# Optimization experiments

Measured on AMD Instinct MI355X. Metric: run time of the kernel, lower is better.

The kernel has to match this reference:

```python
import jax, jax.numpy as jnp
import numpy as np

K = 20  # neighbors per point
EPS = 1e-5


def knn_idx(x, k):
    # x: (B,C,N) -> indices of k nearest neighbors (B,N,k), largest negative sq-dist
    xx = jnp.sum(x * x, axis=1)                      # (B,N)
    inner = jnp.einsum('bcn,bcm->bnm', x, x)         # (B,N,N)
    neg_dist = 2.0 * inner - xx[:, :, None] - xx[:, None, :]
    return jax.lax.top_k(neg_dist, k)[1]             # (B,N,k)


def graph_feature(x, k):
    # x: (B,C,N) -> (B,2C,N,k) = cat(neighbor - center, center)
    idx = knn_idx(x, k)
    gather = jax.vmap(lambda xb, ib: xb[:, ib])(x, idx)      # (B,C,N,k)
    center = jnp.broadcast_to(x[:, :, :, None], gather.shape)
    return jnp.concatenate([gather - center, center], axis=1)


def bn(x, g, b, axes):
    # training-mode batchnorm over given axes; channel axis = 1
    m = jnp.mean(x, axis=axes, keepdims=True)
    v = jnp.var(x, axis=axes, keepdims=True)
    sh = [1] * x.ndim
    sh[1] = x.shape[1]
    return (x - m) * jax.lax.rsqrt(v + EPS) * g.reshape(sh) + b.reshape(sh)


def lrelu(x):
    return jnp.where(x >= 0, x, 0.2 * x)


def edge_block(x, W, g, b, k):
    # EdgeConv: knn-gather -> 1x1 conv -> BN -> LeakyReLU -> max over k
    f = graph_feature(x, k)                          # (B,2C,N,k)
    y = jnp.einsum('oc,bcnk->bonk', W, f)
    return jnp.max(lrelu(bn(y, g, b, (0, 2, 3))), axis=-1)   # (B,O,N)


def conv1d_bn(x, W, g, b):
    y = jnp.einsum('oc,bcn->bon', W, x)
    return lrelu(bn(y, g, b, (0, 2)))


def setup_inputs() -> dict:
    key = jax.random.key(0)
    ks = jax.random.split(key, 12)
    B, N = 4, 4096
    d = {'points': jax.random.normal(ks[0], (B, N, 3), dtype=jnp.float32)}

    def w(k, o, c):
        return jax.random.normal(k, (o, c), dtype=jnp.float32) * (1.0 / np.sqrt(c))

    d['W1'] = w(ks[1], 64, 6);     d['g1'] = jnp.ones(64);  d['b1'] = jnp.zeros(64)
    d['W2'] = w(ks[2], 64, 128);   d['g2'] = jnp.ones(64);  d['b2'] = jnp.zeros(64)
    d['W3'] = w(ks[3], 128, 128);  d['g3'] = jnp.ones(128); d['b3'] = jnp.zeros(128)
    d['W4'] = w(ks[4], 256, 256);  d['g4'] = jnp.ones(256); d['b4'] = jnp.zeros(256)
    d['W5'] = w(ks[5], 512, 512);  d['g5'] = jnp.ones(512); d['b5'] = jnp.zeros(512)
    d['Ws1'] = w(ks[6], 256, 1024); d['gs1'] = jnp.ones(256); d['bs1'] = jnp.zeros(256)
    d['Ws2'] = w(ks[7], 128, 256);  d['gs2'] = jnp.ones(128); d['bs2'] = jnp.zeros(128)
    d['Ws3'] = w(ks[8], 2, 128);    d['bias3'] = jnp.zeros(2)
    return d


def reference(points, W1, g1, b1, W2, g2, b2, W3, g3, b3, W4, g4, b4,
              W5, g5, b5, Ws1, gs1, bs1, Ws2, gs2, bs2, Ws3, bias3):
    x = jnp.transpose(points, (0, 2, 1))             # (B,3,N)
    x1 = edge_block(x, W1, g1, b1, K)                # (B,64,N)
    x2 = edge_block(x1, W2, g2, b2, K)               # (B,64,N)
    x3 = edge_block(x2, W3, g3, b3, K)               # (B,128,N)
    x4 = edge_block(x3, W4, g4, b4, K)               # (B,256,N)
    xc = jnp.concatenate([x1, x2, x3, x4], axis=1)   # (B,512,N)
    x5 = conv1d_bn(xc, W5, g5, b5)                   # (B,512,N)
    g = jnp.broadcast_to(jnp.max(x5, axis=2, keepdims=True), x5.shape)
    feat = jnp.concatenate([xc, g], axis=1)          # (B,1024,N)
    h = conv1d_bn(feat, Ws1, gs1, bs1)               # (B,256,N)
    h = conv1d_bn(h, Ws2, gs2, bs2)                  # (B,128,N)
    return jnp.einsum('oc,bcn->bon', Ws3, h) + bias3[None, :, None]  # (B,2,N)
```

## Files before the change

kernel.cpp:

```cpp
#include <hip/hip_runtime.h>

#define NPTS 4096
#define NB 4
#define KNN 20
#define NCAND 64
#define RANKT 32
#define MROWS (NB*NPTS)

__device__ __forceinline__ float lrelu(float v) { return v >= 0.f ? v : 0.2f * v; }

__device__ __forceinline__ unsigned fkey(float f) {
  unsigned u = __float_as_uint(f);
  return (u & 0x80000000u) ? ~u : (u | 0x80000000u);
}
__device__ __forceinline__ float funkey(unsigned k) {
  unsigned u = (k & 0x80000000u) ? (k ^ 0x80000000u) : ~k;
  return __uint_as_float(u);
}

__global__ __launch_bounds__(256) void sqnorm_k(const float* __restrict__ X, int ldx, int C,
                                                float* __restrict__ xx) {
  int r = blockIdx.x * 256 + threadIdx.x;
  if (r >= MROWS) return;
  const float* row = X + (size_t)r * ldx;
  float s = 0.f;
  for (int c = 0; c < C; ++c) { float v = row[c]; s += v * v; }
  xx[r] = s;
}

__global__ __launch_bounds__(256, 2) void gemm128_k(
    const float* __restrict__ A, int lda,
    const float* __restrict__ B, int ldb, int C,
    float* __restrict__ out, int ldo,
    const float* __restrict__ bias2d, int bstride,
    const float* __restrict__ xxa, const float* __restrict__ xxb) {
  __shared__ float As[32][128];
  __shared__ float Bs[32][128];
  int t = threadIdx.x;
  int tx = t & 15, ty = t >> 4;
  int mbase = blockIdx.x * 128;
  int rbase = blockIdx.y * 128;
  float acc[8][8] = {};
  int lr = t >> 1;
  int lk = (t & 1) * 16;
  const float* pa0 = A + (size_t)(rbase + lr) * lda + lk;
  const float* pb0 = B + (size_t)(mbase + lr) * ldb + lk;
  for (int kc = 0; kc < C; kc += 32) {
    const float* pa = pa0 + kc;
    const float* pb = pb0 + kc;
    #pragma unroll
    for (int j4 = 0; j4 < 4; ++j4) {
      float4 a4 = *(const float4*)(pa + j4 * 4);
      float4 b4 = *(const float4*)(pb + j4 * 4);
      As[lk + j4*4 + 0][lr] = a4.x;
      As[lk + j4*4 + 1][lr] = a4.y;
      As[lk + j4*4 + 2][lr] = a4.z;
      As[lk + j4*4 + 3][lr] = a4.w;
      Bs[lk + j4*4 + 0][lr] = b4.x;
      Bs[lk + j4*4 + 1][lr] = b4.y;
      Bs[lk + j4*4 + 2][lr] = b4.z;
      Bs[lk + j4*4 + 3][lr] = b4.w;
    }
    __syncthreads();
    #pragma unroll
    for (int k = 0; k < 32; ++k) {
      float4 a0 = ((const float4*)As[k])[ty];
      float4 a1 = ((const float4*)As[k])[16 + ty];
      float4 b0 = ((const float4*)Bs[k])[tx];
      float4 b1 = ((const float4*)Bs[k])[16 + tx];
      float av[8] = {a0.x,a0.y,a0.z,a0.w,a1.x,a1.y,a1.z,a1.w};
      float bv[8] = {b0.x,b0.y,b0.z,b0.w,b1.x,b1.y,b1.z,b1.w};
      #pragma unroll
      for (int i = 0; i < 8; ++i)
        #pragma unroll
        for (int j = 0; j < 8; ++j)
          acc[i][j] += av[i] * bv[j];
    }
    __syncthreads();
  }
  #pragma unroll
  for (int ih = 0; ih < 2; ++ih) {
    #pragma unroll
    for (int i4 = 0; i4 < 4; ++i4) {
      int i = ih * 4 + i4;
      int r = rbase + ih * 64 + ty * 4 + i4;
      float xr = xxa ? xxa[r] : 0.f;
      const float* brow = bias2d ? (bias2d + (size_t)(r >> 12) * bstride) : nullptr;
      #pragma unroll
      for (int jh = 0; jh < 2; ++jh) {
        float4 o4;
        #pragma unroll
        for (int j4 = 0; j4 < 4; ++j4) {
          int j = jh * 4 + j4;
          int m = mbase + jh * 64 + tx * 4 + j4;
          float val = acc[i][j];
          if (xxa) val = 2.f * val - xr - xxb[m];
          else if (brow) val += brow[m];
          (&o4.x)[j4] = val;
        }
        *(float4*)&out[(size_t)r * ldo + mbase + jh * 64 + tx * 4] = o4;
      }
    }
  }
}

__global__ __launch_bounds__(256, 2) void dist_tri_k(const float* __restrict__ Xb, int ldx, int C,
                                                     const float* __restrict__ xxb,
                                                     float* __restrict__ D) {
  __shared__ float As[32][128];
  __shared__ float Bs[32][128];
  __shared__ float Ts[32][129];
  int t = threadIdx.x;
  int tx = t & 15, ty = t >> 4;
  int lin = blockIdx.x, bi = 0;
  while (lin >= 32 - bi) { lin -= 32 - bi; ++bi; }
  int bj = bi + lin;
  int rbase = bi * 128;
  int mbase = bj * 128;
  float acc[8][8] = {};
  int lr = t >> 1;
  int lk = (t & 1) * 16;
  const float* pa0 = Xb + (size_t)(rbase + lr) * ldx + lk;
  const float* pb0 = Xb + (size_t)(mbase + lr) * ldx + lk;
  for (int kc = 0; kc < C; kc += 32) {
    const float* pa = pa0 + kc;
    const float* pb = pb0 + kc;
    #pragma unroll
    for (int j4 = 0; j4 < 4; ++j4) {
      float4 a4 = *(const float4*)(pa + j4 * 4);
      float4 b4 = *(const float4*)(pb + j4 * 4);
      As[lk + j4*4 + 0][lr] = a4.x;
      As[lk + j4*4 + 1][lr] = a4.y;
      As[lk + j4*4 + 2][lr] = a4.z;
      As[lk + j4*4 + 3][lr] = a4.w;
      Bs[lk + j4*4 + 0][lr] = b4.x;
      Bs[lk + j4*4 + 1][lr] = b4.y;
      Bs[lk + j4*4 + 2][lr] = b4.z;
      Bs[lk + j4*4 + 3][lr] = b4.w;
    }
    __syncthreads();
    #pragma unroll
    for (int k = 0; k < 32; ++k) {
      float4 a0 = ((const float4*)As[k])[ty];
      float4 a1 = ((const float4*)As[k])[16 + ty];
      float4 b0 = ((const float4*)Bs[k])[tx];
      float4 b1 = ((const float4*)Bs[k])[16 + tx];
      float av[8] = {a0.x,a0.y,a0.z,a0.w,a1.x,a1.y,a1.z,a1.w};
      float bv[8] = {b0.x,b0.y,b0.z,b0.w,b1.x,b1.y,b1.z,b1.w};
      #pragma unroll
      for (int i = 0; i < 8; ++i)
        #pragma unroll
        for (int j = 0; j < 8; ++j)
          acc[i][j] += av[i] * bv[j];
    }
    __syncthreads();
  }
  #pragma unroll
  for (int ih = 0; ih < 2; ++ih) {
    #pragma unroll
    for (int i4 = 0; i4 < 4; ++i4) {
      int i = ih * 4 + i4;
      int r = rbase + ih * 64 + ty * 4 + i4;
      float xr = xxb[r];
      #pragma unroll
      for (int jh = 0; jh < 2; ++jh) {
        float4 o4;
        #pragma unroll
        for (int j4 = 0; j4 < 4; ++j4) {
          int j = jh * 4 + j4;
          int m = mbase + jh * 64 + tx * 4 + j4;
          float val = 2.f * acc[i][j] - xr - xxb[m];
          acc[i][j] = val;
          (&o4.x)[j4] = val;
        }
        *(float4*)&D[(size_t)r * NPTS + mbase + jh * 64 + tx * 4] = o4;
      }
    }
  }
  if (bi != bj) {
    #pragma unroll
    for (int g = 0; g < 4; ++g) {
      __syncthreads();
      #pragma unroll
      for (int jh = 0; jh < 2; ++jh) {
        int mlo = jh * 64 + tx * 4;
        if ((mlo >> 5) == g) {
          #pragma unroll
          for (int i = 0; i < 8; ++i) {
            int r_local = (i >> 2) * 64 + ty * 4 + (i & 3);
            #pragma unroll
            for (int j4 = 0; j4 < 4; ++j4)
              Ts[(mlo & 31) + j4][r_local] = acc[i][jh * 4 + j4];
          }
        }
      }
      __syncthreads();
      int rowg = t >> 3;
      int colb = (t & 7) * 16;
      int mg = mbase + g * 32 + rowg;
      float4* dst = (float4*)&D[(size_t)mg * NPTS + rbase + colb];
      #pragma unroll
      for (int q = 0; q < 4; ++q) {
        float4 vq;
        vq.x = Ts[rowg][colb + q*4 + 0];
        vq.y = Ts[rowg][colb + q*4 + 1];
        vq.z = Ts[rowg][colb + q*4 + 2];
        vq.w = Ts[rowg][colb + q*4 + 3];
        dst[q] = vq;
      }
    }
  }
}

#define HISTN (16*257)

__global__ __launch_bounds__(256) void select_k(const float* __restrict__ D,
                                                int* __restrict__ cand, int b, int n0) {
  __shared__ __align__(16) unsigned keys[NPTS];
  __shared__ __align__(16) int hist[HISTN];
  __shared__ int wtot[4];
  __shared__ unsigned sT;
  __shared__ unsigned sM;
  __shared__ int sR;
  __shared__ int sA;
  __shared__ int sDone;
  __shared__ int sCnt;
  int t = threadIdx.x;
  int wv = t >> 6;
  int lane = t & 63;
  int* hrow = hist + (t & 15) * 257;
  int r = blockIdx.x;
  const float4* drow4 = (const float4*)(D + (size_t)r * NPTS);
  int4 z4 = {0, 0, 0, 0};
  #pragma unroll
  for (int i = 0; i < HISTN/4/256 + 1; ++i) {
    int idx = i * 256 + t;
    if (idx < HISTN/4) ((int4*)hist)[idx] = z4;
  }
  if (t == 0) { sT = 0u; sM = 0u; sR = RANKT; sA = 0; sDone = 0; sCnt = 0; }
  __syncthreads();
  #pragma unroll
  for (int i = 0; i < 4; ++i) {
    float4 d4 = drow4[i*256 + t];
    uint4 k4;
    k4.x = fkey(d4.x); k4.y = fkey(d4.y); k4.z = fkey(d4.z); k4.w = fkey(d4.w);
    ((uint4*)keys)[i*256 + t] = k4;
    atomicAdd(&hrow[k4.x >> 24], 1);
    atomicAdd(&hrow[k4.y >> 24], 1);
    atomicAdd(&hrow[k4.z >> 24], 1);
    atomicAdd(&hrow[k4.w >> 24], 1);
  }
  __syncthreads();
  int done = 0;
  for (int level = 0; level < 4 && !done; ++level) {
    unsigned M = sM, T = sT;
    int R = sR;
    int shift = 24 - 8 * level;
    if (level > 0) {
      #pragma unroll
      for (int i = 0; i < HISTN/4/256 + 1; ++i) {
        int idx = i * 256 + t;
        if (idx < HISTN/4) ((int4*)hist)[idx] = z4;
      }
      __syncthreads();
      #pragma unroll
      for (int i = 0; i < 4; ++i) {
        uint4 k4 = ((uint4*)keys)[i*256 + t];
        if ((k4.x & M) == T) atomicAdd(&hrow[(k4.x >> shift) & 0xffu], 1);
        if ((k4.y & M) == T) atomicAdd(&hrow[(k4.y >> shift) & 0xffu], 1);
        if ((k4.z & M) == T) atomicAdd(&hrow[(k4.z >> shift) & 0xffu], 1);
        if ((k4.w & M) == T) atomicAdd(&hrow[(k4.w >> shift) & 0xffu], 1);
      }
      __syncthreads();
    }
    int h = 0;
    #pragma unroll
    for (int j = 0; j < 16; ++j) h += hist[j * 257 + t];
    int s = h;
    #pragma unroll
    for (int off = 1; off < 64; off <<= 1) {
      int o = __shfl(s, lane + off);
      if (lane + off < 64) s += o;
    }
    if (lane == 0) wtot[wv] = s;
    __syncthreads();
    int aw = 0;
    for (int w = wv + 1; w < 4; ++w) aw += wtot[w];
    int sAbove = (s - h) + aw;
    if (sAbove < R && R <= sAbove + h) {
      unsigned v = (unsigned)t;
      int strictNow = sA + sAbove;
      sT = T | (v << shift);
      sM = M | (0xffu << shift);
      sA = strictNow;
      sR = R - sAbove;
      sDone = (strictNow + h <= NCAND) || (level == 3);
    }
    __syncthreads();
    done = sDone;
  }
  unsigned T = sT;
  int* orow = cand + ((size_t)b * NPTS + n0 + r) * NCAND;
  #pragma unroll
  for (int i = 0; i < 4; ++i) {
    uint4 k4 = ((uint4*)keys)[i*256 + t];
    int mb = 4 * (i*256 + t);
    if (k4.x >= T) { int p = atomicAdd(&sCnt, 1); if (p < NCAND) orow[p] = mb + 0; }
    if (k4.y >= T) { int p = atomicAdd(&sCnt, 1); if (p < NCAND) orow[p] = mb + 1; }
    if (k4.z >= T) { int p = atomicAdd(&sCnt, 1); if (p < NCAND) orow[p] = mb + 2; }
    if (k4.w >= T) { int p = atomicAdd(&sCnt, 1); if (p < NCAND) orow[p] = mb + 3; }
  }
  __syncthreads();
  int c = sCnt; if (c > NCAND) c = NCAND;
  if (t >= c && t < NCAND) orow[t] = 0x7fffffff;
}

__global__ __launch_bounds__(256) void select3_k(const float* __restrict__ X,
                                                 int* __restrict__ cand) {
  __shared__ __align__(16) unsigned keys[NPTS];
  __shared__ __align__(16) int hist[HISTN];
  __shared__ int wtot[4];
  __shared__ unsigned sT;
  __shared__ unsigned sM;
  __shared__ int sR;
  __shared__ int sA;
  __shared__ int sDone;
  __shared__ int sCnt;
  int t = threadIdx.x;
  int wv = t >> 6;
  int lane = t & 63;
  int* hrow = hist + (t & 15) * 257;
  int r = blockIdx.x;
  int b = r >> 12, n = r & 4095;
  const float* xb = X + (size_t)b * NPTS * 3;
  float x0 = xb[n*3+0], x1 = xb[n*3+1], x2 = xb[n*3+2];
  int4 z4 = {0, 0, 0, 0};
  #pragma unroll
  for (int i = 0; i < HISTN/4/256 + 1; ++i) {
    int idx = i * 256 + t;
    if (idx < HISTN/4) ((int4*)hist)[idx] = z4;
  }
  if (t == 0) { sT = 0u; sM = 0u; sR = RANKT; sA = 0; sDone = 0; sCnt = 0; }
  __syncthreads();
  #pragma unroll
  for (int i = 0; i < NPTS/256; ++i) {
    int m = i*256 + t;
    float d0 = x0 - xb[m*3+0];
    float d1 = x1 - xb[m*3+1];
    float d2 = x2 - xb[m*3+2];
    unsigned k = fkey(-(d0*d0 + d1*d1 + d2*d2));
    keys[m] = k;
    atomicAdd(&hrow[k >> 24], 1);
  }
  __syncthreads();
  int done = 0;
  for (int level = 0; level < 4 && !done; ++level) {
    unsigned M = sM, T = sT;
    int R = sR;
    int shift = 24 - 8 * level;
    if (level > 0) {
      #pragma unroll
      for (int i = 0; i < HISTN/4/256 + 1; ++i) {
        int idx = i * 256 + t;
        if (idx < HISTN/4) ((int4*)hist)[idx] = z4;
      }
      __syncthreads();
      #pragma unroll
      for (int i = 0; i < 4; ++i) {
        uint4 k4 = ((uint4*)keys)[i*256 + t];
        if ((k4.x & M) == T) atomicAdd(&hrow[(k4.x >> shift) & 0xffu], 1);
        if ((k4.y & M) == T) atomicAdd(&hrow[(k4.y >> shift) & 0xffu], 1);
        if ((k4.z & M) == T) atomicAdd(&hrow[(k4.z >> shift) & 0xffu], 1);
        if ((k4.w & M) == T) atomicAdd(&hrow[(k4.w >> shift) & 0xffu], 1);
      }
      __syncthreads();
    }
    int h = 0;
    #pragma unroll
    for (int j = 0; j < 16; ++j) h += hist[j * 257 + t];
    int s = h;
    #pragma unroll
    for (int off = 1; off < 64; off <<= 1) {
      int o = __shfl(s, lane + off);
      if (lane + off < 64) s += o;
    }
    if (lane == 0) wtot[wv] = s;
    __syncthreads();
    int aw = 0;
    for (int w = wv + 1; w < 4; ++w) aw += wtot[w];
    int sAbove = (s - h) + aw;
    if (sAbove < R && R <= sAbove + h) {
      unsigned v = (unsigned)t;
      int strictNow = sA + sAbove;
      sT = T | (v << shift);
      sM = M | (0xffu << shift);
      sA = strictNow;
      sR = R - sAbove;
      sDone = (strictNow + h <= NCAND) || (level == 3);
    }
    __syncthreads();
    done = sDone;
  }
  unsigned T = sT;
  int* orow = cand + (size_t)r * NCAND;
  #pragma unroll
  for (int i = 0; i < 4; ++i) {
    uint4 k4 = ((uint4*)keys)[i*256 + t];
    int mb = 4 * (i*256 + t);
    if (k4.x >= T) { int p = atomicAdd(&sCnt, 1); if (p < NCAND) orow[p] = mb + 0; }
    if (k4.y >= T) { int p = atomicAdd(&sCnt, 1); if (p < NCAND) orow[p] = mb + 1; }
    if (k4.z >= T) { int p = atomicAdd(&sCnt, 1); if (p < NCAND) orow[p] = mb + 2; }
    if (k4.w >= T) { int p = atomicAdd(&sCnt, 1); if (p < NCAND) orow[p] = mb + 3; }
  }
  __syncthreads();
  int c = sCnt; if (c > NCAND) c = NCAND;
  if (t >= c && t < NCAND) orow[t] = 0x7fffffff;
}

__global__ __launch_bounds__(256) void refine_k(const float* __restrict__ X, int ldx, int C,
                                                const int* __restrict__ cand,
                                                int* __restrict__ idx) {
  int t = threadIdx.x;
  int lane = t & 63;
  int row = blockIdx.x * 4 + (t >> 6);
  int b = row >> 12, n = row & 4095;
  const float* Xb = X + (size_t)b * NPTS * ldx;
  const float* xn = Xb + (size_t)n * ldx;
  int m = cand[(size_t)row * NCAND + lane];
  double s;
  if (m >= NPTS) {
    s = 1e300;
  } else if (C == 3) {
    const float* xm = Xb + (size_t)m * 3;
    double d0 = (double)xn[0] - xm[0];
    double d1 = (double)xn[1] - xm[1];
    double d2 = (double)xn[2] - xm[2];
    s = d0*d0 + d1*d1 + d2*d2;
  } else {
    const float* xm = Xb + (size_t)m * ldx;
    double s0 = 0, s1 = 0, s2 = 0, s3 = 0;
    for (int c = 0; c < C; c += 4) {
      float4 a = *(const float4*)(xn + c);
      float4 q = *(const float4*)(xm + c);
      double e0 = (double)a.x - q.x; s0 += e0*e0;
      double e1 = (double)a.y - q.y; s1 += e1*e1;
      double e2 = (double)a.z - q.z; s2 += e2*e2;
      double e3 = (double)a.w - q.w; s3 += e3*e3;
    }
    s = (s0 + s1) + (s2 + s3);
  }
  #pragma unroll
  for (int k = 2; k <= 64; k <<= 1) {
    #pragma unroll
    for (int j = k >> 1; j > 0; j >>= 1) {
      double os = __shfl_xor(s, j);
      int om = __shfl_xor(m, j);
      bool up = ((lane & k) == 0);
      bool keepSmall = (((lane & j) == 0) == up);
      bool iGreater = (s > os) || (s == os && m > om);
      if (keepSmall == iGreater) { s = os; m = om; }
    }
  }
  if (lane < KNN) idx[(size_t)row * KNN + lane] = m;
}

__global__ __launch_bounds__(256) void gemm_k(const float* __restrict__ X, int ldx,
                                              const float* __restrict__ W, int ldw,
                                              float* __restrict__ out, int ldo,
                                              const float* __restrict__ bias2d, int bstride,
                                              int C) {
  __shared__ float As[16][66];
  __shared__ float Bs[16][66];
  int t = threadIdx.x;
  int tx = t & 15, ty = t >> 4;
  int obase = blockIdx.x * 64;
  int rbase = blockIdx.y * 64;
  float acc[4][4] = {};
  int kk = t & 15, r0 = t >> 4;
  for (int kc = 0; kc < C; kc += 16) {
    #pragma unroll
    for (int i = 0; i < 4; ++i) {
      int rr = r0 + i * 16;
      float a = 0.f, bv = 0.f;
      if (kc + kk < C) {
        a  = X[(size_t)(rbase + rr) * ldx + kc + kk];
        bv = W[(size_t)(obase + rr) * ldw + kc + kk];
      }
      As[kk][rr] = a;
      Bs[kk][rr] = bv;
    }
    __syncthreads();
    #pragma unroll
    for (int k = 0; k < 16; ++k) {
      float av[4], bv2[4];
      #pragma unroll
      for (int i = 0; i < 4; ++i) { av[i] = As[k][ty + 16*i]; bv2[i] = Bs[k][tx + 16*i]; }
      #pragma unroll
      for (int i = 0; i < 4; ++i)
        #pragma unroll
        for (int j = 0; j < 4; ++j)
          acc[i][j] += av[i] * bv2[j];
    }
    __syncthreads();
  }
  #pragma unroll
  for (int i = 0; i < 4; ++i) {
    int r = rbase + ty + 16*i;
    #pragma unroll
    for (int j = 0; j < 4; ++j) {
      int o = obase + tx + 16*j;
      float val = acc[i][j];
      if (bias2d) val += bias2d[(r >> 12) * bstride + o];
      out[(size_t)r * ldo + o] = val;
    }
  }
}

__global__ __launch_bounds__(256) void prep_w(const float* __restrict__ W,
                                              float* __restrict__ wn, float* __restrict__ wd,
                                              int O, int C) {
  int i = blockIdx.x * 256 + threadIdx.x;
  if (i >= O * C) return;
  int o = i / C, c = i - o * C;
  float nn = W[(size_t)o * 2 * C + c];
  float cc = W[(size_t)o * 2 * C + C + c];
  wn[i] = nn;
  wd[i] = cc - nn;
}

__global__ __launch_bounds__(256) void gather_k(const float* __restrict__ u, const float* __restrict__ v,
                                                const int* __restrict__ idx,
                                                float* __restrict__ mxb, float* __restrict__ mnb,
                                                double* __restrict__ gsum, double* __restrict__ gsq, int O) {
  __shared__ int sidx[16 * KNN];
  int t = threadIdx.x;
  int p0 = blockIdx.x * 16;
  int b = p0 >> 12;
  const int* ib = idx + (size_t)p0 * KNN;
  for (int i = t; i < 16 * KNN; i += 256) sidx[i] = ib[i];
  __syncthreads();
  int o = t & (O - 1);
  int pl = t / O;
  int ppi = 256 / O;
  const float* ub = u + ((size_t)b << 12) * O;
  double S = 0.0, S2 = 0.0;
  for (int p = pl; p < 16; p += ppi) {
    int r = p0 + p;
    float vv = v[(size_t)r * O + o];
    float mx = -3.4e38f, mn = 3.4e38f;
    double su = 0.0, su2 = 0.0;
    #pragma unroll
    for (int k = 0; k < KNN; ++k) {
      int m = sidx[p * KNN + k];
      float uv = ub[(size_t)m * O + o];
      mx = fmaxf(mx, uv);
      mn = fminf(mn, uv);
      double du = uv;
      su += du; su2 += du * du;
    }
    mxb[(size_t)r * O + o] = mx;
    mnb[(size_t)r * O + o] = mn;
    double dv = vv;
    S  += su + (double)KNN * dv;
    S2 += su2 + 2.0 * dv * su + (double)KNN * dv * dv;
  }
  atomicAdd(&gsum[o], S);
  atomicAdd(&gsq[o], S2);
}

__global__ __launch_bounds__(256) void finalize_k(const double* __restrict__ gsum, const double* __restrict__ gsq,
                                                  const float* __restrict__ g, const float* __restrict__ bp,
                                                  float* __restrict__ a, float* __restrict__ bb,
                                                  double invM, int O) {
  int o = blockIdx.x * 256 + threadIdx.x;
  if (o >= O) return;
  double mean = gsum[o] * invM;
  double var = gsq[o] * invM - mean * mean;
  double sc = (double)g[o] / sqrt(var + 1e-5);
  a[o] = (float)sc;
  bb[o] = (float)((double)bp[o] - mean * sc);
}

__global__ __launch_bounds__(256) void edge_out2(const float* __restrict__ v,
                                                 const float* __restrict__ mxb, const float* __restrict__ mnb,
                                                 const float* __restrict__ a, const float* __restrict__ bb,
                                                 float* __restrict__ xc, int coff, int O, int lgO) {
  int i = blockIdx.x * 256 + threadIdx.x;
  int r = i >> lgO, o = i & (O - 1);
  float av = a[o];
  float sel = av >= 0.f ? mxb[i] : mnb[i];
  float val = av * (v[i] + sel) + bb[o];
  xc[(size_t)r * 512 + coff + o] = lrelu(val);
}

__global__ __launch_bounds__(256) void col_stats(const float* __restrict__ y, int ld, int O,
                                                 double* __restrict__ gsum, double* __restrict__ gsq) {
  int t = threadIdx.x;
  int r0 = blockIdx.x * 64;
  double s0 = 0, q0 = 0, s1 = 0, q1 = 0;
  for (int rr = 0; rr < 64; ++rr) {
    const float* row = y + (size_t)(r0 + rr) * ld;
    if (t < O) { double v0 = row[t]; s0 += v0; q0 += v0 * v0; }
    if (O == 512) { double v1 = row[t + 256]; s1 += v1; q1 += v1 * v1; }
  }
  if (t < O) { atomicAdd(&gsum[t], s0); atomicAdd(&gsq[t], q0); }
  if (O == 512) { atomicAdd(&gsum[t + 256], s1); atomicAdd(&gsq[t + 256], q1); }
}

__global__ __launch_bounds__(256) void conv5_max(const float* __restrict__ y,
                                                 const float* __restrict__ a, const float* __restrict__ bb,
                                                 unsigned* __restrict__ gmax) {
  int t = threadIdx.x;
  int b = blockIdx.y;
  int r0 = (b << 12) + blockIdx.x * 64;
  float a0 = a[t], a1 = a[t + 256], b0 = bb[t], b1 = bb[t + 256];
  float m0 = -3.4e38f, m1 = -3.4e38f;
  for (int rr = 0; rr < 64; ++rr) {
    const float* row = y + (size_t)(r0 + rr) * 512;
    float v0 = lrelu(a0 * row[t] + b0);
    float v1 = lrelu(a1 * row[t + 256] + b1);
    m0 = fmaxf(m0, v0);
    m1 = fmaxf(m1, v1);
  }
  atomicMax(&gmax[b * 512 + t], fkey(m0));
  atomicMax(&gmax[b * 512 + t + 256], fkey(m1));
}

__global__ __launch_bounds__(256) void gterm_k(const unsigned* __restrict__ gmax,
                                               const float* __restrict__ Ws1,
                                               float* __restrict__ gt) {
  int b = blockIdx.x, o = threadIdx.x;
  double acc = 0.0;
  for (int c = 0; c < 512; ++c)
    acc += (double)funkey(gmax[b * 512 + c]) * (double)Ws1[(size_t)o * 1024 + 512 + c];
  gt[b * 256 + o] = (float)acc;
}

__global__ __launch_bounds__(256) void bn_apply(const float* __restrict__ y, int ld,
                                                const float* __restrict__ a, const float* __restrict__ bb,
                                                float* __restrict__ out, int ldo, int O) {
  int t = threadIdx.x;
  int o = t & (O - 1);
  int pl = t / O;
  int rpi = 256 / O;
  int r0 = blockIdx.x * 64;
  float av = a[o], bv = bb[o];
  for (int rr = pl; rr < 64; rr += rpi) {
    int r = r0 + rr;
    float val = av * y[(size_t)r * ld + o] + bv;
    out[(size_t)r * ldo + o] = lrelu(val);
  }
}

__global__ __launch_bounds__(256) void final_out(const float* __restrict__ h,
                                                 const float* __restrict__ Ws3,
                                                 const float* __restrict__ bias3,
                                                 float* __restrict__ out) {
  int rr = blockIdx.x * 256 + threadIdx.x;
  if (rr >= MROWS) return;
  int b = rr >> 12, n = rr & 4095;
  const float* row = h + (size_t)rr * 128;
  double a0 = 0.0, a1 = 0.0;
  for (int c = 0; c < 128; ++c) {
    double hv = row[c];
    a0 += hv * (double)Ws3[c];
    a1 += hv * (double)Ws3[128 + c];
  }
  out[((size_t)b * 2) * NPTS + n] = (float)(a0 + (double)bias3[0]);
  out[((size_t)b * 2 + 1) * NPTS + n] = (float)(a1 + (double)bias3[1]);
}

extern "C" void kernel_launch(void* const* d_in, const int* in_sizes, int n_in,
                              void* d_out, int out_size, void* d_ws, size_t ws_size,
                              hipStream_t stream) {
  const float* points = (const float*)d_in[0];
  const float* W1 = (const float*)d_in[1];  const float* g1 = (const float*)d_in[2];  const float* b1 = (const float*)d_in[3];
  const float* W2 = (const float*)d_in[4];  const float* g2 = (const float*)d_in[5];  const float* b2 = (const float*)d_in[6];
  const float* W3 = (const float*)d_in[7];  const float* g3 = (const float*)d_in[8];  const float* b3 = (const float*)d_in[9];
  const float* W4 = (const float*)d_in[10]; const float* g4 = (const float*)d_in[11]; const float* b4 = (const float*)d_in[12];
  const float* W5 = (const float*)d_in[13]; const float* g5 = (const float*)d_in[14]; const float* b5 = (const float*)d_in[15];
  const float* Ws1 = (const float*)d_in[16]; const float* gs1 = (const float*)d_in[17]; const float* bs1 = (const float*)d_in[18];
  const float* Ws2 = (const float*)d_in[19]; const float* gs2 = (const float*)d_in[20]; const float* bs2 = (const float*)d_in[21];
  const float* Ws3 = (const float*)d_in[22]; const float* bias3 = (const float*)d_in[23];

  size_t fixedBytes = (size_t)(MROWS*NCAND*4) + (size_t)(MROWS*KNN*4) + (size_t)(MROWS*4)
                    + 2*(size_t)MROWS*256*4 + (size_t)MROWS*512*4 + 2*(256*128*4)
                    + 8*1024 + 4*1024 + NB*512*4 + NB*256*4 + 64*1024;
  int CH = (ws_size >= (size_t)4096 * NPTS * 4 + fixedBytes) ? 4096 : 2048;

  char* p = (char*)d_ws;
  auto carve = [&](size_t nbytes) -> char* {
    char* q = p;
    p += (nbytes + 255) & ~(size_t)255;
    return q;
  };
  float* big  = (float*)carve((size_t)CH * NPTS * 4);
  int*   candb = (int*)carve((size_t)MROWS * NCAND * 4);
  int*   idxb = (int*)carve((size_t)MROWS * KNN * 4);
  float* xx   = (float*)carve((size_t)MROWS * 4);
  float* u    = (float*)carve((size_t)MROWS * 256 * 4);
  float* v    = (float*)carve((size_t)MROWS * 256 * 4);
  float* xcb  = (float*)carve((size_t)MROWS * 512 * 4);
  float* wn   = (float*)carve(256 * 128 * 4);
  float* wd   = (float*)carve(256 * 128 * 4);
  double* gsum = (double*)carve(512 * 8);
  double* gsq  = (double*)carve(512 * 8);
  float* acoef = (float*)carve(512 * 4);
  float* bcoef = (float*)carve(512 * 4);
  unsigned* gmax = (unsigned*)carve(NB * 512 * 4);
  float* gtermb = (float*)carve(NB * 256 * 4);
  float* h1n = u;
  float* h2n = v;

  auto edge = [&](const float* X, int ldx, int C, int O, int lgO,
                  const float* W, const float* g, const float* bp, int coff) {
    if (C == 3) {
      select3_k<<<MROWS, 256, 0, stream>>>(X, candb);
    } else {
      sqnorm_k<<<MROWS / 256, 256, 0, stream>>>(X, ldx, C, xx);
      if (CH == 4096) {
        for (int b = 0; b < NB; ++b) {
          dist_tri_k<<<528, 256, 0, stream>>>(X + (size_t)b * NPTS * ldx, ldx, C,
                                              xx + b * NPTS, big);
          select_k<<<NPTS, 256, 0, stream>>>(big, candb, b, 0);
        }
      } else {
        for (int b = 0; b < NB; ++b) {
          for (int n0 = 0; n0 < NPTS; n0 += CH) {
            gemm128_k<<<dim3(NPTS / 128, CH / 128), 256, 0, stream>>>(
                X + ((size_t)b * NPTS + n0) * ldx, ldx,
                X + (size_t)b * NPTS * ldx, ldx, C,
                big, NPTS, nullptr, 0,
                xx + b * NPTS + n0, xx + b * NPTS);
            select_k<<<CH, 256, 0, stream>>>(big, candb, b, n0);
          }
        }
      }
    }
    refine_k<<<MROWS / 4, 256, 0, stream>>>(X, ldx, C, candb, idxb);
    prep_w<<<(O * C + 255) / 256, 256, 0, stream>>>(W, wn, wd, O, C);
    if (O >= 256) {
      gemm128_k<<<dim3(O / 128, MROWS / 128), 256, 0, stream>>>(X, ldx, wn, C, C, u, O, nullptr, 0, nullptr, nullptr);
      gemm128_k<<<dim3(O / 128, MROWS / 128), 256, 0, stream>>>(X, ldx, wd, C, C, v, O, nullptr, 0, nullptr, nullptr);
    } else {
      gemm_k<<<dim3(O / 64, MROWS / 64), 256, 0, stream>>>(X, ldx, wn, C, u, O, nullptr, 0, C);
      gemm_k<<<dim3(O / 64, MROWS / 64), 256, 0, stream>>>(X, ldx, wd, C, v, O, nullptr, 0, C);
    }
    hipMemsetAsync(gsum, 0, 512 * 8 * 2, stream);
    float* mxb = big;
    float* mnb = big + (size_t)MROWS * O;
    gather_k<<<MROWS / 16, 256, 0, stream>>>(u, v, idxb, mxb, mnb, gsum, gsq, O);
    finalize_k<<<(O + 255) / 256, 256, 0, stream>>>(gsum, gsq, g, bp, acoef, bcoef,
                                                    1.0 / ((double)MROWS * KNN), O);
    edge_out2<<<(MROWS * O) / 256, 256, 0, stream>>>(v, mxb, mnb, acoef, bcoef, xcb, coff, O, lgO);
  };

  edge(points,    3,   3,  64, 6, W1, g1, b1, 0);
  edge(xcb,       512, 64, 64, 6, W2, g2, b2, 64);
  edge(xcb + 64,  512, 64, 128, 7, W3, g3, b3, 128);
  edge(xcb + 128, 512, 128, 256, 8, W4, g4, b4, 256);

  gemm128_k<<<dim3(4, MROWS / 128), 256, 0, stream>>>(xcb, 512, W5, 512, 512, big, 512, nullptr, 0, nullptr, nullptr);
  hipMemsetAsync(gsum, 0, 512 * 8 * 2, stream);
  col_stats<<<MROWS / 64, 256, 0, stream>>>(big, 512, 512, gsum, gsq);
  finalize_k<<<2, 256, 0, stream>>>(gsum, gsq, g5, b5, acoef, bcoef, 1.0 / MROWS, 512);
  hipMemsetAsync(gmax, 0, NB * 512 * 4, stream);
  conv5_max<<<dim3(NPTS / 64, NB), 256, 0, stream>>>(big, acoef, bcoef, gmax);
  gterm_k<<<NB, 256, 0, stream>>>(gmax, Ws1, gtermb);

  gemm128_k<<<dim3(2, MROWS / 128), 256, 0, stream>>>(xcb, 512, Ws1, 1024, 512, big, 256, gtermb, 256, nullptr, nullptr);
  hipMemsetAsync(gsum, 0, 512 * 8 * 2, stream);
  col_stats<<<MROWS / 64, 256, 0, stream>>>(big, 256, 256, gsum, gsq);
  finalize_k<<<1, 256, 0, stream>>>(gsum, gsq, gs1, bs1, acoef, bcoef, 1.0 / MROWS, 256);
  bn_apply<<<MROWS / 64, 256, 0, stream>>>(big, 256, acoef, bcoef, h1n, 256, 256);

  gemm_k<<<dim3(2, MROWS / 64), 256, 0, stream>>>(h1n, 256, Ws2, 256, big, 128, nullptr, 0, 256);
  hipMemsetAsync(gsum, 0, 512 * 8 * 2, stream);
  col_stats<<<MROWS / 64, 256, 0, stream>>>(big, 128, 128, gsum, gsq);
  finalize_k<<<1, 256, 0, stream>>>(gsum, gsq, gs2, bs2, acoef, bcoef, 1.0 / MROWS, 128);
  bn_apply<<<MROWS / 64, 256, 0, stream>>>(big, 128, acoef, bcoef, h2n, 128, 128);

  final_out<<<MROWS / 256, 256, 0, stream>>>(h2n, Ws3, bias3, (float*)d_out);
}
```

Baseline: 2.041 ms.

## Use 10-bit radix select with fewer sub-histograms; recompute keys in select3

The radix top-k selection changes from 8-bit digits to 10-bit digits (levels 22/12/2/0). This cuts the number of histogram passes needed to isolate the threshold. Sub-histogram replication drops from 16 to 8, and each thread reduces four bins with int4 loads. In select3_k the shared key array is removed and distances are recomputed from the xyz coordinates on every pass, trading extra ALU work and global loads for less LDS use and possibly higher occupancy.

Result: slower. 2.159 ms (+5.8%).

```diff
diff --git a/kernel.cpp b/kernel.cpp
--- a/kernel.cpp
+++ b/kernel.cpp
@@ -7,6 +7,11 @@
 #define RANKT 32
 #define MROWS (NB*NPTS)
 
+#define NBIN 1024
+#define NSUB 8
+#define HPITCH 1028
+#define HISTN (NSUB*HPITCH)
+
 __device__ __forceinline__ float lrelu(float v) { return v >= 0.f ? v : 0.2f * v; }
 
 __device__ __forceinline__ unsigned fkey(float f) {
@@ -16,6 +21,14 @@
 __device__ __forceinline__ float funkey(unsigned k) {
   unsigned u = (k & 0x80000000u) ? (k ^ 0x80000000u) : ~k;
   return __uint_as_float(u);
+}
+
+__device__ __forceinline__ unsigned key3(float x0, float x1, float x2,
+                                         const float* __restrict__ xm) {
+  float d0 = x0 - xm[0];
+  float d1 = x1 - xm[1];
+  float d2 = x2 - xm[2];
+  return fkey(-__fmaf_rn(d0, d0, __fmaf_rn(d1, d1, d2 * d2)));
 }
 
 __global__ __launch_bounds__(256) void sqnorm_k(const float* __restrict__ X, int ldx, int C,
@@ -212,7 +225,44 @@
   }
 }
 
-#define HISTN (16*257)
+#define RADIX_REDUCE_AND_PICK(levelVar)                                           \
+  int h0 = 0, h1 = 0, h2 = 0, h3 = 0;                                             \
+  _Pragma("unroll")                                                               \
+  for (int j = 0; j < NSUB; ++j) {                                                \
+    int4 hq = *(int4*)&hist[j * HPITCH + 4 * t];                                  \
+    h0 += hq.x; h1 += hq.y; h2 += hq.z; h3 += hq.w;                               \
+  }                                                                               \
+  int ht = h0 + h1 + h2 + h3;                                                     \
+  int s = ht;                                                                     \
+  _Pragma("unroll")                                                               \
+  for (int off = 1; off < 64; off <<= 1) {                                        \
+    int o = __shfl(s, lane + off);                                                \
+    if (lane + off < 64) s += o;                                                  \
+  }                                                                               \
+  if (lane == 0) wtot[wv] = s;                                                    \
+  __syncthreads();                                                                \
+  int aw = 0;                                                                     \
+  for (int w = wv + 1; w < 4; ++w) aw += wtot[w];                                 \
+  int Sincl = s + aw;                                                             \
+  int above3 = Sincl - ht;                                                        \
+  int above2 = above3 + h3;                                                       \
+  int above1 = above2 + h2;                                                       \
+  int above0 = above1 + h1;                                                       \
+  int hh[4] = {h0, h1, h2, h3};                                                   \
+  int ab[4] = {above0, above1, above2, above3};                                   \
+  _Pragma("unroll")                                                               \
+  for (int q = 0; q < 4; ++q) {                                                   \
+    if (ab[q] < R && R <= ab[q] + hh[q]) {                                        \
+      unsigned v = (unsigned)(4 * t + q);                                         \
+      int strictNow = sA + ab[q];                                                 \
+      sT = T | (v << shift);                                                      \
+      sM = M | (bmask << shift);                                                  \
+      sA = strictNow;                                                             \
+      sR = R - ab[q];                                                             \
+      sDone = (strictNow + hh[q] <= NCAND) || ((levelVar) == 3);                  \
+    }                                                                             \
+  }                                                                               \
+  __syncthreads();
 
 __global__ __launch_bounds__(256) void select_k(const float* __restrict__ D,
                                                 int* __restrict__ cand, int b, int n0) {
@@ -228,12 +278,12 @@
   int t = threadIdx.x;
   int wv = t >> 6;
   int lane = t & 63;
-  int* hrow = hist + (t & 15) * 257;
+  int* hrow = hist + (t & (NSUB - 1)) * HPITCH;
   int r = blockIdx.x;
   const float4* drow4 = (const float4*)(D + (size_t)r * NPTS);
   int4 z4 = {0, 0, 0, 0};
   #pragma unroll
-  for (int i = 0; i < HISTN/4/256 + 1; ++i) {
+  for (int i = 0; i < (HISTN/4 + 255) / 256; ++i) {
     int idx = i * 256 + t;
     if (idx < HISTN/4) ((int4*)hist)[idx] = z4;
   }
@@ -245,20 +295,21 @@
     uint4 k4;
     k4.x = fkey(d4.x); k4.y = fkey(d4.y); k4.z = fkey(d4.z); k4.w = fkey(d4.w);
     ((uint4*)keys)[i*256 + t] = k4;
-    atomicAdd(&hrow[k4.x >> 24], 1);
-    atomicAdd(&hrow[k4.y >> 24], 1);
-    atomicAdd(&hrow[k4.z >> 24], 1);
-    atomicAdd(&hrow[k4.w >> 24], 1);
+    atomicAdd(&hrow[k4.x >> 22], 1);
+    atomicAdd(&hrow[k4.y >> 22], 1);
+    atomicAdd(&hrow[k4.z >> 22], 1);
+    atomicAdd(&hrow[k4.w >> 22], 1);
   }
   __syncthreads();
   int done = 0;
   for (int level = 0; level < 4 && !done; ++level) {
     unsigned M = sM, T = sT;
     int R = sR;
-    int shift = 24 - 8 * level;
+    int shift = (level < 3) ? (22 - 10 * level) : 0;
+    unsigned bmask = (level < 3) ? 0x3ffu : 0x3u;
     if (level > 0) {
       #pragma unroll
-      for (int i = 0; i < HISTN/4/256 + 1; ++i) {
+      for (int i = 0; i < (HISTN/4 + 255) / 256; ++i) {
         int idx = i * 256 + t;
         if (idx < HISTN/4) ((int4*)hist)[idx] = z4;
       }
@@ -266,37 +317,14 @@
       #pragma unroll
       for (int i = 0; i < 4; ++i) {
         uint4 k4 = ((uint4*)keys)[i*256 + t];
-        if ((k4.x & M) == T) atomicAdd(&hrow[(k4.x >> shift) & 0xffu], 1);
-        if ((k4.y & M) == T) atomicAdd(&hrow[(k4.y >> shift) & 0xffu], 1);
-        if ((k4.z & M) == T) atomicAdd(&hrow[(k4.z >> shift) & 0xffu], 1);
-        if ((k4.w & M) == T) atomicAdd(&hrow[(k4.w >> shift) & 0xffu], 1);
+        if ((k4.x & M) == T) atomicAdd(&hrow[(k4.x >> shift) & bmask], 1);
+        if ((k4.y & M) == T) atomicAdd(&hrow[(k4.y >> shift) & bmask], 1);
+        if ((k4.z & M) == T) atomicAdd(&hrow[(k4.z >> shift) & bmask], 1);
+        if ((k4.w & M) == T) atomicAdd(&hrow[(k4.w >> shift) & bmask], 1);
       }
       __syncthreads();
     }
-    int h = 0;
-    #pragma unroll
-    for (int j = 0; j < 16; ++j) h += hist[j * 257 + t];
-    int s = h;
-    #pragma unroll
-    for (int off = 1; off < 64; off <<= 1) {
-      int o = __shfl(s, lane + off);
-      if (lane + off < 64) s += o;
-    }
-    if (lane == 0) wtot[wv] = s;
-    __syncthreads();
-    int aw = 0;
-    for (int w = wv + 1; w < 4; ++w) aw += wtot[w];
-    int sAbove = (s - h) + aw;
-    if (sAbove < R && R <= sAbove + h) {
-      unsigned v = (unsigned)t;
-      int strictNow = sA + sAbove;
-      sT = T | (v << shift);
-      sM = M | (0xffu << shift);
-      sA = strictNow;
-      sR = R - sAbove;
-      sDone = (strictNow + h <= NCAND) || (level == 3);
-    }
-    __syncthreads();
+    RADIX_REDUCE_AND_PICK(level)
     done = sDone;
   }
   unsigned T = sT;
@@ -317,7 +345,6 @@
 
 __global__ __launch_bounds__(256) void select3_k(const float* __restrict__ X,
                                                  int* __restrict__ cand) {
-  __shared__ __align__(16) unsigned keys[NPTS];
   __shared__ __align__(16) int hist[HISTN];
   __shared__ int wtot[4];
   __shared__ unsigned sT;
@@ -329,88 +356,60 @@
   int t = threadIdx.x;
   int wv = t >> 6;
   int lane = t & 63;
-  int* hrow = hist + (t & 15) * 257;
+  int* hrow = hist + (t & (NSUB - 1)) * HPITCH;
   int r = blockIdx.x;
   int b = r >> 12, n = r & 4095;
   const float* xb = X + (size_t)b * NPTS * 3;
   float x0 = xb[n*3+0], x1 = xb[n*3+1], x2 = xb[n*3+2];
   int4 z4 = {0, 0, 0, 0};
   #pragma unroll
-  for (int i = 0; i < HISTN/4/256 + 1; ++i) {
+  for (int i = 0; i < (HISTN/4 + 255) / 256; ++i) {
     int idx = i * 256 + t;
     if (idx < HISTN/4) ((int4*)hist)[idx] = z4;
   }
   if (t == 0) { sT = 0u; sM = 0u; sR = RANKT; sA = 0; sDone = 0; sCnt = 0; }
   __syncthreads();
   #pragma unroll
-  for (int i = 0; i < NPTS/256; ++i) {
+  for (int i = 0; i < 16; ++i) {
     int m = i*256 + t;
-    float d0 = x0 - xb[m*3+0];
-    float d1 = x1 - xb[m*3+1];
-    float d2 = x2 - xb[m*3+2];
-    unsigned k = fkey(-(d0*d0 + d1*d1 + d2*d2));
-    keys[m] = k;
-    atomicAdd(&hrow[k >> 24], 1);
+    unsigned k = key3(x0, x1, x2, xb + m*3);
+    atomicAdd(&hrow[k >> 22], 1);
   }
   __syncthreads();
   int done = 0;
   for (int level = 0; level < 4 && !done; ++level) {
     unsigned M = sM, T = sT;
     int R = sR;
-    int shift = 24 - 8 * level;
+    int shift = (level < 3) ? (22 - 10 * level) : 0;
+    unsigned bmask = (level < 3) ? 0x3ffu : 0x3u;
     if (level > 0) {
       #pragma unroll
-      for (int i = 0; i < HISTN/4/256 + 1; ++i) {
+      for (int i = 0; i < (HISTN/4 + 255) / 256; ++i) {
         int idx = i * 256 + t;
         if (idx < HISTN/4) ((int4*)hist)[idx] = z4;
       }
       __syncthreads();
       #pragma unroll
-      for (int i = 0; i < 4; ++i) {
-        uint4 k4 = ((uint4*)keys)[i*256 + t];
-        if ((k4.x & M) == T) atomicAdd(&hrow[(k4.x >> shift) & 0xffu], 1);
-        if ((k4.y & M) == T) atomicAdd(&hrow[(k4.y >> shift) & 0xffu], 1);
-        if ((k4.z & M) == T) atomicAdd(&hrow[(k4.z >> shift) & 0xffu], 1);
-        if ((k4.w & M) == T) atomicAdd(&hrow[(k4.w >> shift) & 0xffu], 1);
+      for (int i = 0; i < 16; ++i) {
+        int m = i*256 + t;
+        unsigned k = key3(x0, x1, x2, xb + m*3);
+        if ((k & M) == T) atomicAdd(&hrow[(k >> shift) & bmask], 1);
       }
       __syncthreads();
     }
-    int h = 0;
-    #pragma unroll
-    for (int j = 0; j < 16; ++j) h += hist[j * 257 + t];
-    int s = h;
-    #pragma unroll
-    for (int off = 1; off < 64; off <<= 1) {
-      int o = __shfl(s, lane + off);
-      if (lane + off < 64) s += o;
-    }
-    if (lane == 0) wtot[wv] = s;
-    __syncthreads();
-    int aw = 0;
-    for (int w = wv + 1; w < 4; ++w) aw += wtot[w];
-    int sAbove = (s - h) + aw;
-    if (sAbove < R && R <= sAbove + h) {
-      unsigned v = (unsigned)t;
-      int strictNow = sA + sAbove;
-      sT = T | (v << shift);
-      sM = M | (0xffu << shift);
-      sA = strictNow;
-      sR = R - sAbove;
-      sDone = (strictNow + h <= NCAND) || (level == 3);
-    }
-    __syncthreads();
+    RADIX_REDUCE_AND_PICK(level)
     done = sDone;
   }
   unsigned T = sT;
   int* orow = cand + (size_t)r * NCAND;
   #pragma unroll
-  for (int i = 0; i < 4; ++i) {
-    uint4 k4 = ((uint4*)keys)[i*256 + t];
-    int mb = 4 * (i*256 + t);
-    if (k4.x >= T) { int p = atomicAdd(&sCnt, 1); if (p < NCAND) orow[p] = mb + 0; }
-    if (k4.y >= T) { int p = atomicAdd(&sCnt, 1); if (p < NCAND) orow[p] = mb + 1; }
-    if (k4.z >= T) { int p = atomicAdd(&sCnt, 1); if (p < NCAND) orow[p] = mb + 2; }
-    if (k4.w >= T) { int p = atomicAdd(&sCnt, 1); if (p < NCAND) orow[p] = mb + 3; }
+  for (int i = 0; i < 16; ++i) {
+    int m = i*256 + t;
+    unsigned k = key3(x0, x1, x2, xb + m*3);
+    if (k >= T) {
+      int p = atomicAdd(&sCnt, 1);
+      if (p < NCAND) orow[p] = m;
+    }
   }
   __syncthreads();
   int c = sCnt; if (c > NCAND) c = NCAND;
```

## Fuse BN column stats into GEMM epilogue and merge u/v projection GEMMs

Applied to the files above, without the earlier changes.

Adds an optional epilogue to gemm128_k that accumulates per-column sum and sum-of-squares. It reduces them through shared-memory atomics, then does double atomics to global, which removes the separate col_stats passes over the conv5/seg1/seg2 outputs. The two per-edge-block projection GEMMs (neighbor weight and center-minus-neighbor weight) are merged into one GEMM with 2*O outputs into an interleaved uv buffer. The Ws2 layer is also switched to gemm128_k. Per-thread float partial sums before the double atomics cost some precision, and the wider uv row stride changes the gather access pattern.

New measurement: 2.016 ms. Within noise of the previous version (-1.2%).

```diff
diff --git a/kernel.cpp b/kernel.cpp
--- a/kernel.cpp
+++ b/kernel.cpp
@@ -6,6 +6,7 @@
 #define NCAND 64
 #define RANKT 32
 #define MROWS (NB*NPTS)
+#define HISTN (16*257)
 
 __device__ __forceinline__ float lrelu(float v) { return v >= 0.f ? v : 0.2f * v; }
 
@@ -33,7 +34,8 @@
     const float* __restrict__ B, int ldb, int C,
     float* __restrict__ out, int ldo,
     const float* __restrict__ bias2d, int bstride,
-    const float* __restrict__ xxa, const float* __restrict__ xxb) {
+    const float* __restrict__ xxa, const float* __restrict__ xxb,
+    double* __restrict__ colsum, double* __restrict__ colsq) {
   __shared__ float As[32][128];
   __shared__ float Bs[32][128];
   int t = threadIdx.x;
@@ -78,6 +80,8 @@
     }
     __syncthreads();
   }
+  float psum[8] = {};
+  float psq[8] = {};
   #pragma unroll
   for (int ih = 0; ih < 2; ++ih) {
     #pragma unroll
@@ -96,10 +100,28 @@
           float val = acc[i][j];
           if (xxa) val = 2.f * val - xr - xxb[m];
           else if (brow) val += brow[m];
+          if (colsum) { psum[j] += val; psq[j] += val * val; }
           (&o4.x)[j4] = val;
         }
         *(float4*)&out[(size_t)r * ldo + mbase + jh * 64 + tx * 4] = o4;
       }
+    }
+  }
+  if (colsum) {
+    float* ls = (float*)As;
+    float* lq = (float*)Bs;
+    if (t < 128) { ls[t] = 0.f; lq[t] = 0.f; }
+    __syncthreads();
+    #pragma unroll
+    for (int j = 0; j < 8; ++j) {
+      int cl = (j >> 2) * 64 + tx * 4 + (j & 3);
+      atomicAdd(&ls[cl], psum[j]);
+      atomicAdd(&lq[cl], psq[j]);
+    }
+    __syncthreads();
+    if (t < 128) {
+      atomicAdd(&colsum[mbase + t], (double)ls[t]);
+      atomicAdd(&colsq[mbase + t], (double)lq[t]);
     }
   }
 }
@@ -211,8 +233,6 @@
     }
   }
 }
-
-#define HISTN (16*257)
 
 __global__ __launch_bounds__(256) void select_k(const float* __restrict__ D,
                                                 int* __restrict__ cand, int b, int n0) {
@@ -517,19 +537,19 @@
 }
 
 __global__ __launch_bounds__(256) void prep_w(const float* __restrict__ W,
-                                              float* __restrict__ wn, float* __restrict__ wd,
+                                              float* __restrict__ wuv,
                                               int O, int C) {
   int i = blockIdx.x * 256 + threadIdx.x;
   if (i >= O * C) return;
   int o = i / C, c = i - o * C;
   float nn = W[(size_t)o * 2 * C + c];
   float cc = W[(size_t)o * 2 * C + C + c];
-  wn[i] = nn;
-  wd[i] = cc - nn;
+  wuv[(size_t)o * C + c] = nn;
+  wuv[(size_t)(O + o) * C + c] = cc - nn;
 }
 
 __global__ __launch_bounds__(256) void gather_k(const float* __restrict__ u, const float* __restrict__ v,
-                                                const int* __restrict__ idx,
+                                                int lduv, const int* __restrict__ idx,
                                                 float* __restrict__ mxb, float* __restrict__ mnb,
                                                 double* __restrict__ gsum, double* __restrict__ gsq, int O) {
   __shared__ int sidx[16 * KNN];
@@ -542,20 +562,20 @@
   int o = t & (O - 1);
   int pl = t / O;
   int ppi = 256 / O;
-  const float* ub = u + ((size_t)b << 12) * O;
+  const float* ub = u + ((size_t)b << 12) * lduv;
   double S = 0.0, S2 = 0.0;
   for (int p = pl; p < 16; p += ppi) {
     int r = p0 + p;
-    float vv = v[(size_t)r * O + o];
+    float vv = v[(size_t)r * lduv + o];
     float mx = -3.4e38f, mn = 3.4e38f;
     double su = 0.0, su2 = 0.0;
     #pragma unroll
     for (int k = 0; k < KNN; ++k) {
       int m = sidx[p * KNN + k];
-      float uv = ub[(size_t)m * O + o];
-      mx = fmaxf(mx, uv);
-      mn = fminf(mn, uv);
-      double du = uv;
+      float uvv = ub[(size_t)m * lduv + o];
+      mx = fmaxf(mx, uvv);
+      mn = fminf(mn, uvv);
+      double du = uvv;
       su += du; su2 += du * du;
     }
     mxb[(size_t)r * O + o] = mx;
@@ -581,7 +601,7 @@
   bb[o] = (float)((double)bp[o] - mean * sc);
 }
 
-__global__ __launch_bounds__(256) void edge_out2(const float* __restrict__ v,
+__global__ __launch_bounds__(256) void edge_out2(const float* __restrict__ v, int lduv,
                                                  const float* __restrict__ mxb, const float* __restrict__ mnb,
                                                  const float* __restrict__ a, const float* __restrict__ bb,
                                                  float* __restrict__ xc, int coff, int O, int lgO) {
@@ -589,22 +609,8 @@
   int r = i >> lgO, o = i & (O - 1);
   float av = a[o];
   float sel = av >= 0.f ? mxb[i] : mnb[i];
-  float val = av * (v[i] + sel) + bb[o];
+  float val = av * (v[(size_t)r * lduv + o] + sel) + bb[o];
   xc[(size_t)r * 512 + coff + o] = lrelu(val);
-}
-
-__global__ __launch_bounds__(256) void col_stats(const float* __restrict__ y, int ld, int O,
-                                                 double* __restrict__ gsum, double* __restrict__ gsq) {
-  int t = threadIdx.x;
-  int r0 = blockIdx.x * 64;
-  double s0 = 0, q0 = 0, s1 = 0, q1 = 0;
-  for (int rr = 0; rr < 64; ++rr) {
-    const float* row = y + (size_t)(r0 + rr) * ld;
-    if (t < O) { double v0 = row[t]; s0 += v0; q0 += v0 * v0; }
-    if (O == 512) { double v1 = row[t + 256]; s1 += v1; q1 += v1 * v1; }
-  }
-  if (t < O) { atomicAdd(&gsum[t], s0); atomicAdd(&gsq[t], q0); }
-  if (O == 512) { atomicAdd(&gsum[t + 256], s1); atomicAdd(&gsq[t + 256], q1); }
 }
 
 __global__ __launch_bounds__(256) void conv5_max(const float* __restrict__ y,
@@ -684,7 +690,7 @@
   const float* Ws3 = (const float*)d_in[22]; const float* bias3 = (const float*)d_in[23];
 
   size_t fixedBytes = (size_t)(MROWS*NCAND*4) + (size_t)(MROWS*KNN*4) + (size_t)(MROWS*4)
-                    + 2*(size_t)MROWS*256*4 + (size_t)MROWS*512*4 + 2*(256*128*4)
+                    + (size_t)MROWS*512*4  + (size_t)MROWS*512*4  + (512*256*4)
                     + 8*1024 + 4*1024 + NB*512*4 + NB*256*4 + 64*1024;
   int CH = (ws_size >= (size_t)4096 * NPTS * 4 + fixedBytes) ? 4096 : 2048;
 
@@ -698,19 +704,17 @@
   int*   candb = (int*)carve((size_t)MROWS * NCAND * 4);
   int*   idxb = (int*)carve((size_t)MROWS * KNN * 4);
   float* xx   = (float*)carve((size_t)MROWS * 4);
-  float* u    = (float*)carve((size_t)MROWS * 256 * 4);
-  float* v    = (float*)carve((size_t)MROWS * 256 * 4);
+  float* uv   = (float*)carve((size_t)MROWS * 512 * 4);
   float* xcb  = (float*)carve((size_t)MROWS * 512 * 4);
-  float* wn   = (float*)carve(256 * 128 * 4);
-  float* wd   = (float*)carve(256 * 128 * 4);
+  float* wuv  = (float*)carve(512 * 128 * 4);
   double* gsum = (double*)carve(512 * 8);
   double* gsq  = (double*)carve(512 * 8);
   float* acoef = (float*)carve(512 * 4);
   float* bcoef = (float*)carve(512 * 4);
   unsigned* gmax = (unsigned*)carve(NB * 512 * 4);
   float* gtermb = (float*)carve(NB * 256 * 4);
-  float* h1n = u;
-  float* h2n = v;
+  float* h1n = uv;
+  float* h2n = uv + (size_t)MROWS * 256;
 
   auto edge = [&](const float* X, int ldx, int C, int O, int lgO,
                   const float* W, const float* g, const float* bp, int coff) {
@@ -731,28 +735,27 @@
                 X + ((size_t)b * NPTS + n0) * ldx, ldx,
                 X + (size_t)b * NPTS * ldx, ldx, C,
                 big, NPTS, nullptr, 0,
-                xx + b * NPTS + n0, xx + b * NPTS);
+                xx + b * NPTS + n0, xx + b * NPTS, nullptr, nullptr);
             select_k<<<CH, 256, 0, stream>>>(big, candb, b, n0);
           }
         }
       }
     }
     refine_k<<<MROWS / 4, 256, 0, stream>>>(X, ldx, C, candb, idxb);
-    prep_w<<<(O * C + 255) / 256, 256, 0, stream>>>(W, wn, wd, O, C);
-    if (O >= 256) {
-      gemm128_k<<<dim3(O / 128, MROWS / 128), 256, 0, stream>>>(X, ldx, wn, C, C, u, O, nullptr, 0, nullptr, nullptr);
-      gemm128_k<<<dim3(O / 128, MROWS / 128), 256, 0, stream>>>(X, ldx, wd, C, C, v, O, nullptr, 0, nullptr, nullptr);
-    } else {
-      gemm_k<<<dim3(O / 64, MROWS / 64), 256, 0, stream>>>(X, ldx, wn, C, u, O, nullptr, 0, C);
-      gemm_k<<<dim3(O / 64, MROWS / 64), 256, 0, stream>>>(X, ldx, wd, C, v, O, nullptr, 0, C);
-    }
+    prep_w<<<(O * C + 255) / 256, 256, 0, stream>>>(W, wuv, O, C);
+    int O2 = 2 * O;
+    if (C % 32 == 0)
+      gemm128_k<<<dim3(O2 / 128, MROWS / 128), 256, 0, stream>>>(
+          X, ldx, wuv, C, C, uv, O2, nullptr, 0, nullptr, nullptr, nullptr, nullptr);
+    else
+      gemm_k<<<dim3(O2 / 64, MROWS / 64), 256, 0, stream>>>(X, ldx, wuv, C, uv, O2, nullptr, 0, C);
     hipMemsetAsync(gsum, 0, 512 * 8 * 2, stream);
     float* mxb = big;
     float* mnb = big + (size_t)MROWS * O;
-    gather_k<<<MROWS / 16, 256, 0, stream>>>(u, v, idxb, mxb, mnb, gsum, gsq, O);
+    gather_k<<<MROWS / 16, 256, 0, stream>>>(uv, uv + O, O2, idxb, mxb, mnb, gsum, gsq, O);
     finalize_k<<<(O + 255) / 256, 256, 0, stream>>>(gsum, gsq, g, bp, acoef, bcoef,
                                                     1.0 / ((double)MROWS * KNN), O);
-    edge_out2<<<(MROWS * O) / 256, 256, 0, stream>>>(v, mxb, mnb, acoef, bcoef, xcb, coff, O, lgO);
+    edge_out2<<<(MROWS * O) / 256, 256, 0, stream>>>(uv + O, O2, mxb, mnb, acoef, bcoef, xcb, coff, O, lgO);
   };
 
   edge(points,    3,   3,  64, 6, W1, g1, b1, 0);
@@ -760,23 +763,23 @@
   edge(xcb + 64,  512, 64, 128, 7, W3, g3, b3, 128);
   edge(xcb + 128, 512, 128, 256, 8, W4, g4, b4, 256);
 
-  gemm128_k<<<dim3(4, MROWS / 128), 256, 0, stream>>>(xcb, 512, W5, 512, 512, big, 512, nullptr, 0, nullptr, nullptr);
   hipMemsetAsync(gsum, 0, 512 * 8 * 2, stream);
-  col_stats<<<MROWS / 64, 256, 0, stream>>>(big, 512, 512, gsum, gsq);
+  gemm128_k<<<dim3(4, MROWS / 128), 256, 0, stream>>>(xcb, 512, W5, 512, 512, big, 512,
+                                                      nullptr, 0, nullptr, nullptr, gsum, gsq);
   finalize_k<<<2, 256, 0, stream>>>(gsum, gsq, g5, b5, acoef, bcoef, 1.0 / MROWS, 512);
   hipMemsetAsync(gmax, 0, NB * 512 * 4, stream);
   conv5_max<<<dim3(NPTS / 64, NB), 256, 0, stream>>>(big, acoef, bcoef, gmax);
   gterm_k<<<NB, 256, 0, stream>>>(gmax, Ws1, gtermb);
 
-  gemm128_k<<<dim3(2, MROWS / 128), 256, 0, stream>>>(xcb, 512, Ws1, 1024, 512, big, 256, gtermb, 256, nullptr, nullptr);
   hipMemsetAsync(gsum, 0, 512 * 8 * 2, stream);
-  col_stats<<<MROWS / 64, 256, 0, stream>>>(big, 256, 256, gsum, gsq);
+  gemm128_k<<<dim3(2, MROWS / 128), 256, 0, stream>>>(xcb, 512, Ws1, 1024, 512, big, 256,
+                                                      gtermb, 256, nullptr, nullptr, gsum, gsq);
   finalize_k<<<1, 256, 0, stream>>>(gsum, gsq, gs1, bs1, acoef, bcoef, 1.0 / MROWS, 256);
   bn_apply<<<MROWS / 64, 256, 0, stream>>>(big, 256, acoef, bcoef, h1n, 256, 256);
 
-  gemm_k<<<dim3(2, MROWS / 64), 256, 0, stream>>>(h1n, 256, Ws2, 256, big, 128, nullptr, 0, 256);
   hipMemsetAsync(gsum, 0, 512 * 8 * 2, stream);
-  col_stats<<<MROWS / 64, 256, 0, stream>>>(big, 128, 128, gsum, gsq);
+  gemm128_k<<<dim3(1, MROWS / 128), 256, 0, stream>>>(h1n, 256, Ws2, 256, 256, big, 128,
+                                                      nullptr, 0, nullptr, nullptr, gsum, gsq);
   finalize_k<<<1, 256, 0, stream>>>(gsum, gsq, gs2, bs2, acoef, bcoef, 1.0 / MROWS, 128);
   bn_apply<<<MROWS / 64, 256, 0, stream>>>(big, 128, acoef, bcoef, h2n, 128, 128);
 
```
